# Optimization experiments

Measured on AMD Instinct MI355X. Metric: run time of the kernel, lower is better.

Reference implementation:

```python
import jax, jax.numpy as jnp
import numpy as np

N_NODES = 50000
N_EDGES = 800000
IN_DIM = 128
OUT_DIM = 16
N_HEADS = 4
NEG_SLOPE = 0.01  # jax.nn.leaky_relu default, matches original


def setup_inputs() -> dict:
    key = jax.random.key(0)
    k = jax.random.split(key, 8)
    nodes = jax.random.normal(k[0], (N_NODES, IN_DIM), dtype=jnp.float32)
    edges = jax.random.uniform(k[1], (N_NODES, 1), dtype=jnp.float32)  # node-indexed edge attr (edges[senders] in source)
    senders = jax.random.randint(k[2], (N_EDGES,), 0, N_NODES, dtype=jnp.int32)
    receivers = jax.random.randint(k[3], (N_EDGES,), 0, N_NODES, dtype=jnp.int32)
    W = jax.random.normal(k[4], (N_HEADS * OUT_DIM, IN_DIM), dtype=jnp.float32) / np.sqrt(IN_DIM)
    b = jnp.zeros((N_HEADS * OUT_DIM,), dtype=jnp.float32)
    attn_W = jax.random.normal(k[5], (N_HEADS, 2 * OUT_DIM + 1), dtype=jnp.float32) / np.sqrt(2 * OUT_DIM + 1)
    attn_b = jnp.zeros((N_HEADS,), dtype=jnp.float32)
    return dict(nodes=nodes, edges=edges, senders=senders, receivers=receivers,
                W=W, b=b, attn_W=attn_W, attn_b=attn_b)


def _segment_softmax(logits, seg, num_segments):
    # logits: [E, H, 1]; softmax over edges sharing the same receiver
    m = jax.ops.segment_max(logits, seg, num_segments=num_segments)
    e = jnp.exp(logits - m[seg])
    s = jax.ops.segment_sum(e, seg, num_segments=num_segments)
    return e / s[seg]


def reference(nodes, edges, senders, receivers, W, b, attn_W, attn_b):
    n = nodes.shape[0]
    h = (nodes @ W.T + b).reshape(n, N_HEADS, OUT_DIM)       # [N, H, D]
    sent = h[senders]                                        # [E, H, D]
    recv = h[receivers]                                      # [E, H, D]
    sent_e = jnp.tile(edges[senders], (1, N_HEADS))[..., None]  # [E, H, 1]
    feat = jnp.concatenate([sent, recv, sent_e], axis=-1)    # [E, H, 2D+1]
    logits = (jnp.einsum('ehd,hd->eh', feat, attn_W) + attn_b)[..., None]  # [E, H, 1]
    logits = jax.nn.leaky_relu(logits, NEG_SLOPE)
    logits = logits * jnp.sum(sent_e)                        # scalar scaling as in source
    att = _segment_softmax(logits, receivers, n)             # [E, H, 1]
    msg = sent * att                                         # [E, H, D]
    out = jax.ops.segment_sum(msg, receivers, num_segments=n)  # [N, H, D]
    out = jax.nn.leaky_relu(out, NEG_SLOPE)                  # last=False branch
    return out.reshape(n, N_HEADS * OUT_DIM)
```

## Files before the change

kernel.cpp:

```cpp
#include <hip/hip_runtime.h>
#include <math.h>

#define N_NODES 50000
#define N_EDGES 800000
#define IN_DIM 128
#define OUT_DIM 16
#define N_HEADS 4
#define HID 64
#define AW_COLS 33
#define GN 16
#define GEMM_BLK ((N_NODES + GN - 1) / GN)
#define HE 16
#define HBLK ((N_EDGES + 256 * HE - 1) / (256 * HE))
#define MAXDEG 64

__global__ __launch_bounds__(256, 4) void gemm_hist(
    const float* __restrict__ nodes, const float* __restrict__ W,
    const float* __restrict__ b, const float* __restrict__ attn_W,
    const float* __restrict__ attn_b, const float* __restrict__ edges,
    float* __restrict__ h, double* __restrict__ z_src, double* __restrict__ z_dst,
    const int* __restrict__ senders, const int* __restrict__ receivers,
    int* __restrict__ counts, int* __restrict__ srt_padded,
    double* __restrict__ Ssum) {
    __shared__ float sW[HID * IN_DIM];
    __shared__ float sN[GN * IN_DIM];
    int t = threadIdx.x;

    if (blockIdx.x < HBLK) {
        double* red = (double*)sN;
        int base = blockIdx.x * 256 * HE + t;
        double sp = 0.0;
        #pragma unroll
        for (int j = 0; j < HE; ++j) {
            int e = base + j * 256;
            if (e < N_EDGES) {
                int r = receivers[e];
                int rank = atomicAdd(&counts[r], 1);
                if (rank < MAXDEG)
                    srt_padded[r * MAXDEG + rank] = senders[e];
                sp += (double)edges[senders[e]];
            }
        }
        red[t] = sp;
        __syncthreads();
        for (int off = 128; off > 0; off >>= 1) {
            if (t < off) red[t] += red[t + off];
            __syncthreads();
        }
        if (t == 0) atomicAdd(Ssum, red[0]);
    } else {
        for (int i4 = t; i4 < HID * IN_DIM / 4; i4 += 256) {
            int o = i4 >> 5, kq = i4 & 31;
            float4 v = ((const float4*)W)[i4];
            *(float4*)&sW[o * IN_DIM + (((kq + o) & 31) << 2)] = v;
        }
        int node0 = (blockIdx.x - HBLK) * GN;
        for (int i4 = t; i4 < GN * IN_DIM / 4; i4 += 256) {
            int ln = i4 >> 5;
            int n = node0 + ln;
            float4 v = (n < N_NODES) ? ((const float4*)nodes)[(long long)n * (IN_DIM / 4) + (i4 & 31)]
                                     : make_float4(0.f, 0.f, 0.f, 0.f);
            *(float4*)&sN[i4 << 2] = v;
        }
        __syncthreads();
        int w = t >> 6, l = t & 63;
        int half = l >> 5;
        int o2 = l & 31;
        int nwbase = w * 4 + half * 2;
        double acc0[2], acc1[2];
        double b0 = (double)b[o2], b1 = (double)b[o2 + 32];
        #pragma unroll
        for (int j = 0; j < 2; ++j) { acc0[j] = b0; acc1[j] = b1; }
        const float* wrow0 = &sW[o2 * IN_DIM];
        const float* wrow1 = &sW[(o2 + 32) * IN_DIM];
        const float* nbase = &sN[nwbase * IN_DIM];
        int rot0 = (o2 & 31) << 2;
        float4 wv0 = *(const float4*)&wrow0[rot0];
        float4 wv1 = *(const float4*)&wrow1[rot0];
        float4 nva = *(const float4*)&nbase[0];
        float4 nvb = *(const float4*)&nbase[IN_DIM];
        for (int kq = 0; kq < 32; ++kq) {
            int kn = (kq + 1) & 31;
            int rotn = ((kn + o2) & 31) << 2;
            float4 wv0n = *(const float4*)&wrow0[rotn];
            float4 wv1n = *(const float4*)&wrow1[rotn];
            float4 nvan = *(const float4*)&nbase[kn << 2];
            float4 nvbn = *(const float4*)&nbase[IN_DIM + (kn << 2)];
            double w0x = (double)wv0.x, w0y = (double)wv0.y, w0z = (double)wv0.z, w0w = (double)wv0.w;
            double w1x = (double)wv1.x, w1y = (double)wv1.y, w1z = (double)wv1.z, w1w = (double)wv1.w;
            {
                double nx = (double)nva.x, ny = (double)nva.y;
                double nz = (double)nva.z, nw = (double)nva.w;
                acc0[0] += w0x * nx; acc0[0] += w0y * ny;
                acc0[0] += w0z * nz; acc0[0] += w0w * nw;
                acc1[0] += w1x * nx; acc1[0] += w1y * ny;
                acc1[0] += w1z * nz; acc1[0] += w1w * nw;
            }
            {
                double nx = (double)nvb.x, ny = (double)nvb.y;
                double nz = (double)nvb.z, nw = (double)nvb.w;
                acc0[1] += w0x * nx; acc0[1] += w0y * ny;
                acc0[1] += w0z * nz; acc0[1] += w0w * nw;
                acc1[1] += w1x * nx; acc1[1] += w1y * ny;
                acc1[1] += w1z * nz; acc1[1] += w1w * nw;
            }
            wv0 = wv0n; wv1 = wv1n; nva = nvan; nvb = nvbn;
        }
        int hd0 = o2 >> 4, d = o2 & 15;
        int hd1 = hd0 + 2;
        double aw00 = (double)attn_W[hd0 * AW_COLS + d];
        double aw01 = (double)attn_W[hd0 * AW_COLS + OUT_DIM + d];
        double aw10 = (double)attn_W[hd1 * AW_COLS + d];
        double aw11 = (double)attn_W[hd1 * AW_COLS + OUT_DIM + d];
        double wE0 = (double)attn_W[hd0 * AW_COLS + 2 * OUT_DIM];
        double wE1 = (double)attn_W[hd1 * AW_COLS + 2 * OUT_DIM];
        double bb0 = (double)attn_b[hd0], bb1 = (double)attn_b[hd1];
        #pragma unroll
        for (int j = 0; j < 2; ++j) {
            int n = node0 + nwbase + j;
            if (n >= N_NODES) continue;
            float hf0 = (float)acc0[j];
            float hf1 = (float)acc1[j];
            h[(long long)n * HID + o2] = hf0;
            h[(long long)n * HID + o2 + 32] = hf1;
            double c00 = (double)hf0 * aw00;
            double c01 = (double)hf0 * aw01;
            double c10 = (double)hf1 * aw10;
            double c11 = (double)hf1 * aw11;
            #pragma unroll
            for (int k = 1; k <= 8; k <<= 1) {
                c00 += __shfl_xor(c00, k, 64);
                c01 += __shfl_xor(c01, k, 64);
                c10 += __shfl_xor(c10, k, 64);
                c11 += __shfl_xor(c11, k, 64);
            }
            if (d == 0) {
                double se = (double)edges[n];
                z_src[n * N_HEADS + hd0] = c00 + se * wE0;
                z_dst[n * N_HEADS + hd0] = c01 + bb0;
                z_src[n * N_HEADS + hd1] = c10 + se * wE1;
                z_dst[n * N_HEADS + hd1] = c11 + bb1;
            }
        }
    }
}

__global__ __launch_bounds__(256, 8) void node_fused(
    const float* __restrict__ h, const double* __restrict__ z_src,
    const double* __restrict__ z_dst,
    const int* __restrict__ srt_padded, const int* __restrict__ counts,
    const double* __restrict__ Ssum, float* __restrict__ out) {
    int w = threadIdx.x >> 6;
    int lane = threadIdx.x & 63;
    int nA = blockIdx.x * 8 + w * 2;
    int nB = nA + 1;
    int hd = lane >> 4, q = lane & 15;

    int degA = counts[nA]; if (degA > MAXDEG) degA = MAXDEG;
    int degB = counts[nB]; if (degB > MAXDEG) degB = MAXDEG;
    double S = 4.0 * Ssum[0];
    double zdA = z_dst[nA * N_HEADS + hd];
    double zdB = z_dst[nB * N_HEADS + hd];

    int sA[4], sB[4];
    #pragma unroll
    for (int j = 0; j < 4; ++j) {
        int ei = q + 16 * j;
        sA[j] = (ei < degA) ? srt_padded[nA * MAXDEG + ei] : 0;
        sB[j] = (ei < degB) ? srt_padded[nB * MAXDEG + ei] : 0;
    }
    float yA[4], yB[4];
    #pragma unroll
    for (int j = 0; j < 4; ++j) {
        int ei = q + 16 * j;
        yA[j] = -INFINITY;
        yB[j] = -INFINITY;
        if (ei < degA) {
            double yy = z_src[sA[j] * N_HEADS + hd] + zdA;
            yy = yy > 0.0 ? yy : 0.01 * yy;
            yA[j] = (float)yy;
        }
        if (ei < degB) {
            double yy = z_src[sB[j] * N_HEADS + hd] + zdB;
            yy = yy > 0.0 ? yy : 0.01 * yy;
            yB[j] = (float)yy;
        }
    }
    float mA = fmaxf(fmaxf(yA[0], yA[1]), fmaxf(yA[2], yA[3]));
    float mB = fmaxf(fmaxf(yB[0], yB[1]), fmaxf(yB[2], yB[3]));
    #pragma unroll
    for (int k = 1; k <= 8; k <<= 1) {
        mA = fmaxf(mA, __shfl_xor(mA, k, 64));
        mB = fmaxf(mB, __shfl_xor(mB, k, 64));
    }
    float evA[4], evB[4];
    float dA = 0.f, dB = 0.f;
    #pragma unroll
    for (int j = 0; j < 4; ++j) {
        evA[j] = (yA[j] == -INFINITY) ? 0.f
               : __expf((float)(S * ((double)yA[j] - (double)mA)));
        dA += evA[j];
        evB[j] = (yB[j] == -INFINITY) ? 0.f
               : __expf((float)(S * ((double)yB[j] - (double)mB)));
        dB += evB[j];
    }
    #pragma unroll
    for (int k = 1; k <= 8; k <<= 1) {
        dA += __shfl_xor(dA, k, 64);
        dB += __shfl_xor(dB, k, 64);
    }
    float accA = 0.f;
    #pragma unroll
    for (int j = 0; j < 4; ++j) {
        unsigned long long mk = __ballot(evA[j] != 0.f);
        unsigned um = (unsigned)((mk | (mk >> 16) | (mk >> 32) | (mk >> 48)) & 0xFFFFull);
        while (um) {
            int qq = __builtin_ctz(um);
            um &= um - 1;
            int src = (lane & 48) | qq;
            float evv = __shfl(evA[j], src, 64);
            int sj = __shfl(sA[j], src, 64);
            if (evv != 0.f)
                accA = fmaf(evv, h[sj * HID + lane], accA);
        }
    }
    float accB = 0.f;
    #pragma unroll
    for (int j = 0; j < 4; ++j) {
        unsigned long long mk = __ballot(evB[j] != 0.f);
        unsigned um = (unsigned)((mk | (mk >> 16) | (mk >> 32) | (mk >> 48)) & 0xFFFFull);
        while (um) {
            int qq = __builtin_ctz(um);
            um &= um - 1;
            int src = (lane & 48) | qq;
            float evv = __shfl(evB[j], src, 64);
            int sj = __shfl(sB[j], src, 64);
            if (evv != 0.f)
                accB = fmaf(evv, h[sj * HID + lane], accB);
        }
    }
    float rA = (dA > 0.f) ? accA / dA : 0.f;
    float rB = (dB > 0.f) ? accB / dB : 0.f;
    out[nA * HID + lane] = rA > 0.f ? rA : 0.01f * rA;
    out[nB * HID + lane] = rB > 0.f ? rB : 0.01f * rB;
}

static inline char* ws_take(char*& p, size_t bytes) {
    char* cur = p;
    p += (bytes + 255) & ~(size_t)255;
    return cur;
}

extern "C" void kernel_launch(void* const* d_in, const int* in_sizes, int n_in,
                              void* d_out, int out_size, void* d_ws, size_t ws_size,
                              hipStream_t stream) {
    const float* nodes     = (const float*)d_in[0];
    const float* edges     = (const float*)d_in[1];
    const int*   senders   = (const int*)d_in[2];
    const int*   receivers = (const int*)d_in[3];
    const float* W         = (const float*)d_in[4];
    const float* b         = (const float*)d_in[5];
    const float* attn_W    = (const float*)d_in[6];
    const float* attn_b    = (const float*)d_in[7];
    float* out = (float*)d_out;

    char* p = (char*)d_ws;
    float*  h          = (float*)ws_take(p, sizeof(float) * N_NODES * HID);
    double* z_src      = (double*)ws_take(p, sizeof(double) * N_NODES * N_HEADS);
    double* z_dst      = (double*)ws_take(p, sizeof(double) * N_NODES * N_HEADS);
    int*    counts     = (int*)ws_take(p, sizeof(int) * N_NODES);
    char*   zpad       = ws_take(p, 256);
    double* Ssum       = (double*)zpad;
    int*    srt_padded = (int*)ws_take(p, sizeof(int) * (size_t)N_NODES * MAXDEG);

    hipMemsetAsync(counts, 0, ((sizeof(int) * N_NODES + 255) & ~(size_t)255) + 256, stream);

    gemm_hist<<<HBLK + GEMM_BLK, 256, 0, stream>>>(
        nodes, W, b, attn_W, attn_b, edges, h, z_src, z_dst,
        senders, receivers, counts, srt_padded, Ssum);
    node_fused<<<(N_NODES + 7) / 8, 256, 0, stream>>>(
        h, z_src, z_dst, srt_padded, counts, Ssum, out);
}
```

Measured before the change: 159.1 us.

## Restructure GEMM into 4x4 register tiles with split-K across waves

Each thread now computes a 4x4 block of outputs over a K slice of 32, and the four waves each take a quarter of K. Partial sums are reduced through LDS, and h is staged in LDS before being written with coalesced float4 stores. The goal is more FMA work per LDS load in the FP64 GEMM and fewer scattered global writes. In exchange it adds extra barriers and LDS scratch traffic, drops the N_NODES bounds checks (valid only because 50000 divides by 16), and uses more registers for 16 double accumulators.

```diff
diff --git a/kernel.cpp b/kernel.cpp
--- a/kernel.cpp
+++ b/kernel.cpp
@@ -56,56 +56,81 @@
         }
         int node0 = (blockIdx.x - HBLK) * GN;
         for (int i4 = t; i4 < GN * IN_DIM / 4; i4 += 256) {
-            int ln = i4 >> 5;
-            int n = node0 + ln;
-            float4 v = (n < N_NODES) ? ((const float4*)nodes)[(long long)n * (IN_DIM / 4) + (i4 & 31)]
-                                     : make_float4(0.f, 0.f, 0.f, 0.f);
-            *(float4*)&sN[i4 << 2] = v;
-        }
-        __syncthreads();
+            int ln = i4 >> 5, kq = i4 & 31;
+            float4 v = ((const float4*)nodes)[(long long)(node0 + ln) * (IN_DIM / 4) + kq];
+            *(float4*)&sN[ln * IN_DIM + (((kq + ln) & 31) << 2)] = v;
+        }
+        __syncthreads();
+
         int w = t >> 6, l = t & 63;
+        int og = l & 15;
+        int ng = l >> 4;
+        int kbase = w * 8;
+
+        double acc[4][4];
+        #pragma unroll
+        for (int j = 0; j < 4; ++j)
+            #pragma unroll
+            for (int i = 0; i < 4; ++i) acc[j][i] = 0.0;
+
+        #pragma unroll
+        for (int s = 0; s < 8; ++s) {
+            int kq = kbase + s;
+            float4 wq[4], xq[4];
+            #pragma unroll
+            for (int j = 0; j < 4; ++j) {
+                int o = og + 16 * j;
+                wq[j] = *(const float4*)&sW[o * IN_DIM + (((kq + o) & 31) << 2)];
+            }
+            #pragma unroll
+            for (int i = 0; i < 4; ++i) {
+                int n = ng + 4 * i;
+                xq[i] = *(const float4*)&sN[n * IN_DIM + (((kq + n) & 31) << 2)];
+            }
+            #pragma unroll
+            for (int j = 0; j < 4; ++j) {
+                double wx = (double)wq[j].x, wy = (double)wq[j].y;
+                double wz = (double)wq[j].z, ww = (double)wq[j].w;
+                #pragma unroll
+                for (int i = 0; i < 4; ++i) {
+                    double nx = (double)xq[i].x, ny = (double)xq[i].y;
+                    double nz = (double)xq[i].z, nw = (double)xq[i].w;
+                    acc[j][i] += wx * nx; acc[j][i] += wy * ny;
+                    acc[j][i] += wz * nz; acc[j][i] += ww * nw;
+                }
+            }
+        }
+        __syncthreads();
+
+        double* scr = (double*)sW;
+        if (w > 0) {
+            double* dst = &scr[((w - 1) * 64 + l) * 17];
+            #pragma unroll
+            for (int j = 0; j < 4; ++j)
+                #pragma unroll
+                for (int i = 0; i < 4; ++i) dst[j * 4 + i] = acc[j][i];
+        }
+        __syncthreads();
+        float* h_lds = (float*)sN;
+        if (w == 0) {
+            #pragma unroll
+            for (int j = 0; j < 4; ++j) {
+                double bj = (double)b[og + 16 * j];
+                #pragma unroll
+                for (int i = 0; i < 4; ++i) {
+                    double sum = bj + acc[j][i];
+                    sum += scr[(0 * 64 + l) * 17 + j * 4 + i];
+                    sum += scr[(1 * 64 + l) * 17 + j * 4 + i];
+                    sum += scr[(2 * 64 + l) * 17 + j * 4 + i];
+                    h_lds[(ng + 4 * i) * HID + og + 16 * j] = (float)sum;
+                }
+            }
+        }
+        __syncthreads();
+
         int half = l >> 5;
         int o2 = l & 31;
         int nwbase = w * 4 + half * 2;
-        double acc0[2], acc1[2];
-        double b0 = (double)b[o2], b1 = (double)b[o2 + 32];
-        #pragma unroll
-        for (int j = 0; j < 2; ++j) { acc0[j] = b0; acc1[j] = b1; }
-        const float* wrow0 = &sW[o2 * IN_DIM];
-        const float* wrow1 = &sW[(o2 + 32) * IN_DIM];
-        const float* nbase = &sN[nwbase * IN_DIM];
-        int rot0 = (o2 & 31) << 2;
-        float4 wv0 = *(const float4*)&wrow0[rot0];
-        float4 wv1 = *(const float4*)&wrow1[rot0];
-        float4 nva = *(const float4*)&nbase[0];
-        float4 nvb = *(const float4*)&nbase[IN_DIM];
-        for (int kq = 0; kq < 32; ++kq) {
-            int kn = (kq + 1) & 31;
-            int rotn = ((kn + o2) & 31) << 2;
-            float4 wv0n = *(const float4*)&wrow0[rotn];
-            float4 wv1n = *(const float4*)&wrow1[rotn];
-            float4 nvan = *(const float4*)&nbase[kn << 2];
-            float4 nvbn = *(const float4*)&nbase[IN_DIM + (kn << 2)];
-            double w0x = (double)wv0.x, w0y = (double)wv0.y, w0z = (double)wv0.z, w0w = (double)wv0.w;
-            double w1x = (double)wv1.x, w1y = (double)wv1.y, w1z = (double)wv1.z, w1w = (double)wv1.w;
-            {
-                double nx = (double)nva.x, ny = (double)nva.y;
-                double nz = (double)nva.z, nw = (double)nva.w;
-                acc0[0] += w0x * nx; acc0[0] += w0y * ny;
-                acc0[0] += w0z * nz; acc0[0] += w0w * nw;
-                acc1[0] += w1x * nx; acc1[0] += w1y * ny;
-                acc1[0] += w1z * nz; acc1[0] += w1w * nw;
-            }
-            {
-                double nx = (double)nvb.x, ny = (double)nvb.y;
-                double nz = (double)nvb.z, nw = (double)nvb.w;
-                acc0[1] += w0x * nx; acc0[1] += w0y * ny;
-                acc0[1] += w0z * nz; acc0[1] += w0w * nw;
-                acc1[1] += w1x * nx; acc1[1] += w1y * ny;
-                acc1[1] += w1z * nz; acc1[1] += w1w * nw;
-            }
-            wv0 = wv0n; wv1 = wv1n; nva = nvan; nvb = nvbn;
-        }
         int hd0 = o2 >> 4, d = o2 & 15;
         int hd1 = hd0 + 2;
         double aw00 = (double)attn_W[hd0 * AW_COLS + d];
@@ -117,12 +142,10 @@
         double bb0 = (double)attn_b[hd0], bb1 = (double)attn_b[hd1];
         #pragma unroll
         for (int j = 0; j < 2; ++j) {
-            int n = node0 + nwbase + j;
-            if (n >= N_NODES) continue;
-            float hf0 = (float)acc0[j];
-            float hf1 = (float)acc1[j];
-            h[(long long)n * HID + o2] = hf0;
-            h[(long long)n * HID + o2 + 32] = hf1;
+            int nl = nwbase + j;
+            int n = node0 + nl;
+            float hf0 = h_lds[nl * HID + o2];
+            float hf1 = h_lds[nl * HID + o2 + 32];
             double c00 = (double)hf0 * aw00;
             double c01 = (double)hf0 * aw01;
             double c10 = (double)hf1 * aw10;
@@ -142,6 +165,7 @@
                 z_dst[n * N_HEADS + hd1] = c11 + bb1;
             }
         }
+        ((float4*)h)[(long long)node0 * (HID / 4) + t] = ((const float4*)h_lds)[t];
     }
 }
 
```

Result: faster. 155.1 us (-2.5%).
